# Kernel optimization log

Hardware: AMD Instinct MI355X
Metric: run time of the kernel (lower is better)

Reference implementation:

```python
import jax, jax.numpy as jnp
import numpy as np


def _iterative_pinv(mat, n_iter=6):
    # mat: [b, h, m, m]
    m = mat.shape[-1]
    I = jnp.eye(m, dtype=mat.dtype)
    # global (over all batch/heads) scaling, matching torch.max over full tensor
    init_coef = jnp.max(jnp.sum(jnp.abs(mat), axis=-2)) * jnp.max(jnp.sum(jnp.abs(mat), axis=-1))
    out = jnp.swapaxes(mat, -2, -1) / init_coef
    for _ in range(n_iter):
        mo = jnp.matmul(mat, out)          # [b,h,m,m]
        term1 = 7.0 * I - mo
        term2 = 15.0 * I - jnp.matmul(mo, term1)
        term3 = 13.0 * I - jnp.matmul(mo, term2)
        out = 0.25 * jnp.matmul(out, term3)
    return out


def _landmarks(x, m):
    # x: [b, h, s, d] -> segment means [b, h, m, d]
    b, h, s, d = x.shape
    l = s // m
    return x.reshape(b, h, m, l, d).mean(axis=-2)


def setup_inputs() -> dict:
    key = jax.random.key(0)
    kq, kk, kv = jax.random.split(key, 3)
    shape = (4, 12, 4096, 64)
    return {
        "query": jax.random.normal(kq, shape, dtype=jnp.float32),
        "key": jax.random.normal(kk, shape, dtype=jnp.float32),
        "value": jax.random.normal(kv, shape, dtype=jnp.float32),
        "num_landmarks": 64,
    }


def reference(query, key, value, num_landmarks):
    b, h, s, d = query.shape
    scale = 1.0 / jnp.sqrt(jnp.asarray(d, dtype=query.dtype))
    q_lm = _landmarks(query, num_landmarks)   # [b,h,m,d]
    k_lm = _landmarks(key, num_landmarks)     # [b,h,m,d]
    # F_tilde: [b,h,s,m]
    F_tilde = jax.nn.softmax(jnp.einsum('bhsd,bhmd->bhsm', query, k_lm) * scale, axis=-1)
    # A_tilde: pinv of [b,h,m,m]
    A_tilde = _iterative_pinv(
        jax.nn.softmax(jnp.einsum('bhnd,bhmd->bhnm', q_lm, k_lm) * scale, axis=-1))
    # B_tilde: [b,h,m,s]
    B_tilde = jax.nn.softmax(jnp.einsum('bhmd,bhsd->bhms', q_lm, key) * scale, axis=-1)
    # out = F_tilde @ (A_tilde @ (B_tilde @ value))  -> [b,h,s,d]
    bv = jnp.matmul(B_tilde, value)        # [b,h,m,d]
    abv = jnp.matmul(A_tilde, bv)          # [b,h,m,d]
    return jnp.matmul(F_tilde, abv)        # [b,h,s,d]
```

## Files before the change

### kernel.cpp

```cpp
#include <hip/hip_runtime.h>
#include <math.h>

#define BH 48
#define Ss 4096
#define Dd 64
#define Mm 64
#define NCH 16
#define SCALE 0.125f
#define PLN 4096

typedef unsigned int u32;
typedef unsigned short u16;
typedef __attribute__((ext_vector_type(8))) short short8;
typedef __attribute__((ext_vector_type(4))) float floatx4;

union FRAG { uint4 u; short8 s; };

#define MFMA(a,b,c) __builtin_amdgcn_mfma_f32_16x16x32_bf16(a,b,c,0,0,0)

__device__ __forceinline__ u32 pack2_hi(float a, float b) {
    return (__float_as_uint(a) >> 16) | (__float_as_uint(b) & 0xFFFF0000u);
}
__device__ __forceinline__ float trunc_bf(float a) {
    return __uint_as_float(__float_as_uint(a) & 0xFFFF0000u);
}
__device__ __forceinline__ void split1(float v, u16& h, u16& l) {
    u32 u = __float_as_uint(v);
    h = (u16)(u >> 16);
    float r = v - __uint_as_float(u & 0xFFFF0000u);
    l = (u16)(__float_as_uint(r) >> 16);
}
__device__ __forceinline__ void split8(const float* v, short8& h, short8& l) {
    FRAG H, L;
    float r[8];
#pragma unroll
    for (int i = 0; i < 8; i++) r[i] = v[i] - trunc_bf(v[i]);
    H.u.x = pack2_hi(v[0], v[1]); H.u.y = pack2_hi(v[2], v[3]);
    H.u.z = pack2_hi(v[4], v[5]); H.u.w = pack2_hi(v[6], v[7]);
    L.u.x = pack2_hi(r[0], r[1]); L.u.y = pack2_hi(r[2], r[3]);
    L.u.z = pack2_hi(r[4], r[5]); L.u.w = pack2_hi(r[6], r[7]);
    h = H.s; l = L.s;
}
__device__ __forceinline__ int swz(int row, int col) {
    return row * 64 + ((((col >> 3) ^ (row & 7)) << 3) | (col & 7));
}

__global__ __launch_bounds__(256) void k_landmarks(const float* __restrict__ Q,
                                                   const float* __restrict__ Kg,
                                                   float* __restrict__ qlm,
                                                   float* __restrict__ klm,
                                                   u16* __restrict__ qlmh, u16* __restrict__ qlml,
                                                   u16* __restrict__ klmh, u16* __restrict__ klml) {
    int g = blockIdx.x, bh = blockIdx.y;
    int t = threadIdx.x;
    int seg = t >> 4, d4 = t & 15;
    int m = g * 16 + seg;
    const float* src = blockIdx.z ? Kg : Q;
    float* dst = blockIdx.z ? klm : qlm;
    u16* dh = blockIdx.z ? klmh : qlmh;
    u16* dl = blockIdx.z ? klml : qlml;
    const float* base = src + ((size_t)bh * Ss + (size_t)m * 64) * Dd + d4 * 4;
    float4 acc = make_float4(0.f, 0.f, 0.f, 0.f);
#pragma unroll
    for (int l = 0; l < 64; l++) {
        float4 v = *(const float4*)(base + (size_t)l * Dd);
        acc.x += v.x; acc.y += v.y; acc.z += v.z; acc.w += v.w;
    }
    acc.x *= (1.f / 64.f); acc.y *= (1.f / 64.f);
    acc.z *= (1.f / 64.f); acc.w *= (1.f / 64.f);
    int idx = (bh * Mm + m) * Dd + d4 * 4;
    *(float4*)(dst + idx) = acc;
    float vv[4] = {acc.x, acc.y, acc.z, acc.w};
    u16 hh[4], ll[4];
#pragma unroll
    for (int i = 0; i < 4; i++) split1(vv[i], hh[i], ll[i]);
    *(uint2*)(dh + idx) = make_uint2((u32)hh[0] | ((u32)hh[1] << 16), (u32)hh[2] | ((u32)hh[3] << 16));
    *(uint2*)(dl + idx) = make_uint2((u32)ll[0] | ((u32)ll[1] << 16), (u32)ll[2] | ((u32)ll[3] << 16));
}

__global__ __launch_bounds__(256) void k_lmsm(const float* __restrict__ qlm,
                                              const float* __restrict__ klm,
                                              float* __restrict__ smat,
                                              unsigned int* __restrict__ coef) {
    int bh = blockIdx.x, t = threadIdx.x;
    __shared__ float kl[Mm * Dd];
    __shared__ float ql[Mm * Dd];
    __shared__ float Lp[Mm][Mm + 1];
    const float4* kb = (const float4*)(klm + bh * Mm * Dd);
    const float4* qb = (const float4*)(qlm + bh * Mm * Dd);
    for (int i = t; i < Mm * Dd / 4; i += 256) {
        ((float4*)kl)[i] = kb[i];
        ((float4*)ql)[i] = qb[i];
    }
    __syncthreads();
    int n = t >> 2, c = t & 3;
    float p[16];
#pragma unroll
    for (int jj = 0; jj < 16; jj++) {
        int m = c * 16 + jj;
        float s = 0.f;
#pragma unroll
        for (int d4 = 0; d4 < 16; d4++) {
            int d = (((d4 + c * 4) & 15)) * 4;
            float4 kv = *(const float4*)(kl + m * Dd + d);
            float4 qv = *(const float4*)(ql + n * Dd + d);
            s += qv.x * kv.x + qv.y * kv.y + qv.z * kv.z + qv.w * kv.w;
        }
        p[jj] = s * SCALE;
    }
    float mx = -INFINITY;
#pragma unroll
    for (int jj = 0; jj < 16; jj++) mx = fmaxf(mx, p[jj]);
    mx = fmaxf(mx, __shfl_xor(mx, 1));
    mx = fmaxf(mx, __shfl_xor(mx, 2));
    float den = 0.f;
#pragma unroll
    for (int jj = 0; jj < 16; jj++) { p[jj] = __expf(p[jj] - mx); den += p[jj]; }
    den += __shfl_xor(den, 1);
    den += __shfl_xor(den, 2);
    float inv = 1.0f / den;
#pragma unroll
    for (int jj = 0; jj < 16; jj++) Lp[n][c * 16 + jj] = p[jj] * inv;
    __syncthreads();
    float* sg = smat + bh * Mm * Mm;
    for (int i = t; i < Mm * Mm; i += 256) sg[i] = Lp[i >> 6][i & 63];
    if (t < Mm) {
        float cs = 0.f;
#pragma unroll
        for (int nn = 0; nn < Mm; nn++) cs += Lp[nn][t];
#pragma unroll
        for (int off = 1; off < 64; off <<= 1) cs = fmaxf(cs, __shfl_xor(cs, off));
        if (t == 0) atomicMax(coef + 0, __float_as_uint(cs));
    } else if (t < 2 * Mm) {
        int nn = t - Mm; float rs = 0.f;
#pragma unroll
        for (int m = 0; m < Mm; m++) rs += Lp[nn][m];
#pragma unroll
        for (int off = 1; off < 64; off <<= 1) rs = fmaxf(rs, __shfl_xor(rs, off));
        if (t == Mm) atomicMax(coef + 1, __float_as_uint(rs));
    }
}

__device__ __forceinline__ void pinv_pass(const u16* __restrict__ Ah, const u16* __restrict__ Al,
                                          const u16* __restrict__ Bph, const u16* __restrict__ Bpl,
                                          u16* __restrict__ Oh, u16* __restrict__ Ol,
                                          int w, int c, int hi,
                                          float diag, float sgn, float scl) {
    short8 bfh[2], bfl[2];
#pragma unroll
    for (int ks = 0; ks < 2; ks++) {
        bfh[ks] = *(const short8*)&Bph[swz(w * 16 + c, ks * 32 + hi * 8)];
        bfl[ks] = *(const short8*)&Bpl[swz(w * 16 + c, ks * 32 + hi * 8)];
    }
    int j = w * 16 + c;
#pragma unroll
    for (int ta = 0; ta < 4; ta++) {
        floatx4 acc = (floatx4){0.f, 0.f, 0.f, 0.f};
#pragma unroll
        for (int ks = 0; ks < 2; ks++) {
            short8 afh = *(const short8*)&Ah[swz(ta * 16 + c, ks * 32 + hi * 8)];
            short8 afl = *(const short8*)&Al[swz(ta * 16 + c, ks * 32 + hi * 8)];
            acc = MFMA(afh, bfh[ks], acc);
            acc = MFMA(afl, bfh[ks], acc);
            acc = MFMA(afh, bfl[ks], acc);
        }
        u16 oh[4], ol[4];
#pragma unroll
        for (int r = 0; r < 4; r++) {
            int i = ta * 16 + hi * 4 + r;
            float v = scl * (((i == j) ? diag : 0.f) + sgn * acc[r]);
            split1(v, oh[r], ol[r]);
        }
        int o0 = swz(j, ta * 16 + hi * 4);
        *(u32*)&Oh[o0]     = (u32)oh[0] | ((u32)oh[1] << 16);
        *(u32*)&Oh[o0 + 2] = (u32)oh[2] | ((u32)oh[3] << 16);
        *(u32*)&Ol[o0]     = (u32)ol[0] | ((u32)ol[1] << 16);
        *(u32*)&Ol[o0 + 2] = (u32)ol[2] | ((u32)ol[3] << 16);
    }
}

__global__ __launch_bounds__(256) void k_pinv(const float* __restrict__ smat,
                                              const unsigned int* __restrict__ coef,
                                              float* __restrict__ atil) {
    extern __shared__ u16 P[];
    u16* FaH  = P;             u16* FaL  = P + PLN;
    u16* FxcH = P + 2 * PLN;   u16* FxcL = P + 3 * PLN;
    u16* X0H  = P + 4 * PLN;   u16* X0L  = P + 5 * PLN;
    u16* X1H  = P + 6 * PLN;   u16* X1L  = P + 7 * PLN;
    u16* T1H  = P + 8 * PLN;   u16* T1L  = P + 9 * PLN;
    u16* T2H  = P + 10 * PLN;  u16* T2L  = P + 11 * PLN;
    int bh = blockIdx.x, t = threadIdx.x;
    int w = t >> 6, l = t & 63, c = l & 15, hi = l >> 4;
    float inv = 1.0f / (__uint_as_float(coef[0]) * __uint_as_float(coef[1]));
    {
        int r = t >> 2, kq = (t & 3) * 16;
        const float* ar = smat + bh * 4096 + r * 64 + kq;
        float v[16];
#pragma unroll
        for (int q = 0; q < 4; q++) {
            float4 x = *(const float4*)(ar + q * 4);
            v[q * 4 + 0] = x.x; v[q * 4 + 1] = x.y; v[q * 4 + 2] = x.z; v[q * 4 + 3] = x.w;
        }
        short8 h0, l0, h1, l1;
        split8(v, h0, l0); split8(v + 8, h1, l1);
        *(short8*)&FaH[swz(r, kq)] = h0;     *(short8*)&FaH[swz(r, kq + 8)] = h1;
        *(short8*)&FaL[swz(r, kq)] = l0;     *(short8*)&FaL[swz(r, kq + 8)] = l1;
        float vs[16];
#pragma unroll
        for (int q = 0; q < 16; q++) vs[q] = v[q] * inv;
        split8(vs, h0, l0); split8(vs + 8, h1, l1);
        *(short8*)&FxcH[swz(r, kq)] = h0;    *(short8*)&FxcH[swz(r, kq + 8)] = h1;
        *(short8*)&FxcL[swz(r, kq)] = l0;    *(short8*)&FxcL[swz(r, kq + 8)] = l1;
#pragma unroll
        for (int q = 0; q < 16; q++) {
            u16 h, lo; split1(vs[q], h, lo);
            X0H[swz(kq + q, r)] = h;
            X0L[swz(kq + q, r)] = lo;
        }
    }
    __syncthreads();
    u16 *xrH = X0H, *xrL = X0L, *moH = X1H, *moL = X1L;
    for (int it = 0; it < 6; it++) {
        pinv_pass(FxcH, FxcL, FaH, FaL, moH, moL, w, c, hi, 0.f, 1.f, 1.f);
        pinv_pass(FaH, FaL, FxcH, FxcL, T1H, T1L, w, c, hi, 7.f, -1.f, 1.f);
        __syncthreads();
        pinv_pass(moH, moL, T1H, T1L, T2H, T2L, w, c, hi, 15.f, -1.f, 1.f);
        __syncthreads();
        pinv_pass(moH, moL, T2H, T2L, T1H, T1L, w, c, hi, 13.f, -1.f, 1.f);
        __syncthreads();
        pinv_pass(T1H, T1L, xrH, xrL, moH, moL, w, c, hi, 0.f, 1.f, 0.25f);
        pinv_pass(xrH, xrL, T1H, T1L, FxcH, FxcL, w, c, hi, 0.f, 1.f, 0.25f);
        __syncthreads();
        u16* th = xrH; xrH = moH; moH = th;
        u16* tl = xrL; xrL = moL; moL = tl;
    }
    {
        int i = t >> 2, j0 = (t & 3) * 16;
        FRAG h0, l0, h1, l1;
        h0.s = *(const short8*)&xrH[swz(i, j0)];
        l0.s = *(const short8*)&xrL[swz(i, j0)];
        h1.s = *(const short8*)&xrH[swz(i, j0 + 8)];
        l1.s = *(const short8*)&xrL[swz(i, j0 + 8)];
        float* ob = atil + bh * 4096 + i * 64 + j0;
#pragma unroll
        for (int q = 0; q < 8; q++) {
            ob[q]     = __uint_as_float(((u32)(u16)h0.s[q]) << 16) + __uint_as_float(((u32)(u16)l0.s[q]) << 16);
            ob[q + 8] = __uint_as_float(((u32)(u16)h1.s[q]) << 16) + __uint_as_float(((u32)(u16)l1.s[q]) << 16);
        }
    }
}

__global__ __launch_bounds__(256) void k_bvp(const float* __restrict__ Kg,
                                             const float* __restrict__ Vg,
                                             const u16* __restrict__ qlmh,
                                             const u16* __restrict__ qlml,
                                             float* __restrict__ pnum,
                                             float* __restrict__ pden) {
    __shared__ __align__(16) u16 Pb[2][4096];
    __shared__ __align__(16) u16 vt[2][4096];
    __shared__ __align__(16) float tmp[64 * 68];
    int ch = blockIdx.x, bh = blockIdx.y;
    int t = threadIdx.x, w = t >> 6, l = t & 63, c = l & 15, hi = l >> 4;
    const float* Kbh = Kg + (size_t)bh * Ss * Dd;
    const float* Vbh = Vg + (size_t)bh * Ss * Dd;
    const u16* qh = qlmh + bh * Mm * Dd;
    const u16* ql = qlml + bh * Mm * Dd;
    floatx4 pvC[4];
    float denacc[16];
#pragma unroll
    for (int i = 0; i < 4; i++) pvC[i] = (floatx4){0.f, 0.f, 0.f, 0.f};
#pragma unroll
    for (int i = 0; i < 16; i++) denacc[i] = 0.f;

    for (int tile = 0; tile < 4; ++tile) {
        int s0 = ch * 256 + tile * 64;
        __syncthreads();
        {
            int sl = t >> 2, q = (t & 3) * 16;
            const float4* vp = (const float4*)(Vbh + (size_t)(s0 + sl) * Dd + q);
            float4* dp = (float4*)(tmp + sl * 68 + q);
#pragma unroll
            for (int qq = 0; qq < 4; qq++) dp[qq] = vp[qq];
        }
        {
            int srow = s0 + w * 16 + c;
            const float* kp = Kbh + (size_t)srow * Dd + hi * 8;
            short8 kbh[2], kbl[2];
#pragma unroll
            for (int ks = 0; ks < 2; ks++) {
                float kv[8];
                float4 a = *(const float4*)(kp + ks * 32);
                float4 b = *(const float4*)(kp + ks * 32 + 4);
                kv[0] = a.x; kv[1] = a.y; kv[2] = a.z; kv[3] = a.w;
                kv[4] = b.x; kv[5] = b.y; kv[6] = b.z; kv[7] = b.w;
                split8(kv, kbh[ks], kbl[ks]);
            }
            floatx4 qkC[4];
#pragma unroll
            for (int i = 0; i < 4; i++) qkC[i] = (floatx4){0.f, 0.f, 0.f, 0.f};
#pragma unroll
            for (int mt = 0; mt < 4; mt++) {
#pragma unroll
                for (int ks = 0; ks < 2; ks++) {
                    short8 aH = *(const short8*)&qh[(mt * 16 + c) * 64 + ks * 32 + hi * 8];
                    short8 aL = *(const short8*)&ql[(mt * 16 + c) * 64 + ks * 32 + hi * 8];
                    qkC[mt] = MFMA(aH, kbh[ks], qkC[mt]);
                    qkC[mt] = MFMA(aL, kbh[ks], qkC[mt]);
                    qkC[mt] = MFMA(aH, kbl[ks], qkC[mt]);
                }
            }
#pragma unroll
            for (int mt = 0; mt < 4; mt++) {
#pragma unroll
                for (int r = 0; r < 4; r++) {
                    float pv = __expf(qkC[mt][r] * SCALE);
                    denacc[mt * 4 + r] += pv;
                    int m = mt * 16 + hi * 4 + r;
                    u16 h, lo; split1(pv, h, lo);
                    Pb[0][swz(m, w * 16 + c)] = h;
                    Pb[1][swz(m, w * 16 + c)] = lo;
                }
            }
        }
        __syncthreads();
        {
            int d = t >> 2, sg = t & 3;
            float v[16];
#pragma unroll
            for (int j = 0; j < 16; j++) v[j] = tmp[(sg * 16 + j) * 68 + d];
            short8 h0, l0, h1, l1;
            split8(v, h0, l0); split8(v + 8, h1, l1);
            *(short8*)&vt[0][swz(d, sg * 16)] = h0;
            *(short8*)&vt[0][swz(d, sg * 16 + 8)] = h1;
            *(short8*)&vt[1][swz(d, sg * 16)] = l0;
            *(short8*)&vt[1][swz(d, sg * 16 + 8)] = l1;
        }
        __syncthreads();
#pragma unroll
        for (int ks = 0; ks < 2; ks++) {
            short8 pah = *(const short8*)&Pb[0][swz(w * 16 + c, ks * 32 + hi * 8)];
            short8 pal = *(const short8*)&Pb[1][swz(w * 16 + c, ks * 32 + hi * 8)];
#pragma unroll
            for (int dt = 0; dt < 4; dt++) {
                short8 vh = *(const short8*)&vt[0][swz(dt * 16 + c, ks * 32 + hi * 8)];
                short8 vl = *(const short8*)&vt[1][swz(dt * 16 + c, ks * 32 + hi * 8)];
                pvC[dt] = MFMA(pah, vh, pvC[dt]);
                pvC[dt] = MFMA(pal, vh, pvC[dt]);
                pvC[dt] = MFMA(pah, vl, pvC[dt]);
            }
        }
    }
    float* nb = pnum + (size_t)(bh * NCH + ch) * 4096;
#pragma unroll
    for (int dt = 0; dt < 4; dt++)
#pragma unroll
        for (int r = 0; r < 4; r++)
            nb[(w * 16 + hi * 4 + r) * 64 + dt * 16 + c] = pvC[dt][r];
#pragma unroll
    for (int i = 0; i < 16; i++) {
        float v = denacc[i];
        v += __shfl_xor(v, 1); v += __shfl_xor(v, 2);
        v += __shfl_xor(v, 4); v += __shfl_xor(v, 8);
        denacc[i] = v;
    }
    if (c == 0) {
        float* db = pden + (size_t)((bh * NCH + ch) * 4 + w) * 64;
#pragma unroll
        for (int mt = 0; mt < 4; mt++)
#pragma unroll
            for (int r = 0; r < 4; r++)
                db[mt * 16 + hi * 4 + r] = denacc[mt * 4 + r];
    }
}

__global__ __launch_bounds__(256) void k_bvc(const float* __restrict__ pnum,
                                             const float* __restrict__ pden,
                                             const float* __restrict__ atil,
                                             u16* __restrict__ abvh,
                                             u16* __restrict__ abvl) {
    int bh = blockIdx.x, t = threadIdx.x;
    __shared__ float bvs[Mm][Dd + 1];
    __shared__ float Ams[Mm * (Mm + 1)];
    const float* ab = atil + bh * Mm * Mm;
    for (int i = t; i < Mm * Mm; i += 256) Ams[(i >> 6) * 65 + (i & 63)] = ab[i];
    int m = t >> 2, c = t & 3, d0 = c * 16;
    float den = 0.f;
    const float* db = pden + (size_t)bh * NCH * 4 * 64;
#pragma unroll
    for (int i = 0; i < NCH * 4; i++) den += db[i * 64 + m];
    float acc[16];
#pragma unroll
    for (int i = 0; i < 16; i++) acc[i] = 0.f;
    const float* nb = pnum + (size_t)bh * NCH * 4096;
    for (int ch = 0; ch < NCH; ch++) {
        const float4* pa = (const float4*)(nb + ch * 4096 + m * 64 + d0);
#pragma unroll
        for (int q = 0; q < 4; q++) {
            float4 v = pa[q];
            acc[q * 4 + 0] += v.x; acc[q * 4 + 1] += v.y;
            acc[q * 4 + 2] += v.z; acc[q * 4 + 3] += v.w;
        }
    }
    float inv = 1.0f / den;
#pragma unroll
    for (int ii = 0; ii < 16; ii++) bvs[m][d0 + ii] = acc[ii] * inv;
    __syncthreads();
    int j = t & 63, i0 = (t >> 6) << 4;
    float outv[16];
#pragma unroll
    for (int ii = 0; ii < 16; ii++) outv[ii] = 0.f;
#pragma unroll
    for (int k = 0; k < Mm; k++) {
        float bk = bvs[k][j];
#pragma unroll
        for (int ii = 0; ii < 16; ii++) outv[ii] += Ams[(i0 + ii) * 65 + k] * bk;
    }
    u16* oh = abvh + bh * 4096;
    u16* ol = abvl + bh * 4096;
#pragma unroll
    for (int ii = 0; ii < 16; ii++) {
        u16 h, lo; split1(outv[ii], h, lo);
        oh[j * 64 + i0 + ii] = h;
        ol[j * 64 + i0 + ii] = lo;
    }
}

__global__ __launch_bounds__(256) void k_fout(const float* __restrict__ Qg,
                                              const u16* __restrict__ klmh,
                                              const u16* __restrict__ klml,
                                              const u16* __restrict__ abvh,
                                              const u16* __restrict__ abvl,
                                              float* __restrict__ Og) {
    __shared__ __align__(16) u16 Pw[4][2][1024];
    int st = blockIdx.x, bh = blockIdx.y;
    int t = threadIdx.x, w = t >> 6, l = t & 63, c = l & 15, hi = l >> 4;
    int srow = st * 64 + w * 16 + c;
    short8 qah[2], qal[2];
    {
        const float* qp = Qg + ((size_t)bh * Ss + srow) * Dd + hi * 8;
#pragma unroll
        for (int ks = 0; ks < 2; ks++) {
            float qv[8];
            float4 a = *(const float4*)(qp + ks * 32);
            float4 b = *(const float4*)(qp + ks * 32 + 4);
            qv[0] = a.x; qv[1] = a.y; qv[2] = a.z; qv[3] = a.w;
            qv[4] = b.x; qv[5] = b.y; qv[6] = b.z; qv[7] = b.w;
            split8(qv, qah[ks], qal[ks]);
        }
    }
    const u16* kh = klmh + bh * 4096;
    const u16* kl_ = klml + bh * 4096;
    floatx4 qkC[4];
#pragma unroll
    for (int i = 0; i < 4; i++) qkC[i] = (floatx4){0.f, 0.f, 0.f, 0.f};
#pragma unroll
    for (int mt = 0; mt < 4; mt++) {
#pragma unroll
        for (int ks = 0; ks < 2; ks++) {
            short8 bH = *(const short8*)&kh[(mt * 16 + c) * 64 + ks * 32 + hi * 8];
            short8 bL = *(const short8*)&kl_[(mt * 16 + c) * 64 + ks * 32 + hi * 8];
            qkC[mt] = MFMA(qah[ks], bH, qkC[mt]);
            qkC[mt] = MFMA(qal[ks], bH, qkC[mt]);
            qkC[mt] = MFMA(qah[ks], bL, qkC[mt]);
        }
    }
    float p[16], dsum[4];
#pragma unroll
    for (int r = 0; r < 4; r++) dsum[r] = 0.f;
#pragma unroll
    for (int mt = 0; mt < 4; mt++)
#pragma unroll
        for (int r = 0; r < 4; r++) {
            float pv = __expf(qkC[mt][r] * SCALE);
            p[mt * 4 + r] = pv;
            dsum[r] += pv;
        }
#pragma unroll
    for (int r = 0; r < 4; r++) {
        float v = dsum[r];
        v += __shfl_xor(v, 1); v += __shfl_xor(v, 2);
        v += __shfl_xor(v, 4); v += __shfl_xor(v, 8);
        dsum[r] = 1.0f / v;
    }
#pragma unroll
    for (int mt = 0; mt < 4; mt++)
#pragma unroll
        for (int r = 0; r < 4; r++) {
            float pv = p[mt * 4 + r] * dsum[r];
            u16 h, lo; split1(pv, h, lo);
            Pw[w][0][swz(hi * 4 + r, mt * 16 + c)] = h;
            Pw[w][1][swz(hi * 4 + r, mt * 16 + c)] = lo;
        }
    __syncthreads();
    short8 pah[2], pal[2];
#pragma unroll
    for (int ks = 0; ks < 2; ks++) {
        pah[ks] = *(const short8*)&Pw[w][0][swz(c, ks * 32 + hi * 8)];
        pal[ks] = *(const short8*)&Pw[w][1][swz(c, ks * 32 + hi * 8)];
    }
    const u16* ah = abvh + bh * 4096;
    const u16* al = abvl + bh * 4096;
    floatx4 oC[4];
#pragma unroll
    for (int i = 0; i < 4; i++) oC[i] = (floatx4){0.f, 0.f, 0.f, 0.f};
#pragma unroll
    for (int dt = 0; dt < 4; dt++) {
#pragma unroll
        for (int ks = 0; ks < 2; ks++) {
            short8 bH = *(const short8*)&ah[(dt * 16 + c) * 64 + ks * 32 + hi * 8];
            short8 bL = *(const short8*)&al[(dt * 16 + c) * 64 + ks * 32 + hi * 8];
            oC[dt] = MFMA(pah[ks], bH, oC[dt]);
            oC[dt] = MFMA(pal[ks], bH, oC[dt]);
            oC[dt] = MFMA(pah[ks], bL, oC[dt]);
        }
    }
    float* ob = Og + ((size_t)bh * Ss + st * 64 + w * 16) * Dd;
#pragma unroll
    for (int dt = 0; dt < 4; dt++)
#pragma unroll
        for (int r = 0; r < 4; r++)
            ob[(hi * 4 + r) * 64 + dt * 16 + c] = oC[dt][r];
}

extern "C" void kernel_launch(void* const* d_in, const int* in_sizes, int n_in,
                              void* d_out, int out_size, void* d_ws, size_t ws_size,
                              hipStream_t stream) {
    const float* Q = (const float*)d_in[0];
    const float* K = (const float*)d_in[1];
    const float* V = (const float*)d_in[2];
    float* out = (float*)d_out;
    float* ws = (float*)d_ws;
    unsigned int* coef = (unsigned int*)d_ws;
    float* qlm  = ws + 16;
    float* klm  = qlm  + BH * Mm * Dd;
    float* smat = klm  + BH * Mm * Dd;
    float* atil = smat + BH * Mm * Mm;
    float* pnum = atil + BH * Mm * Mm;
    float* pden = pnum + (size_t)BH * NCH * Mm * Dd;
    u16* ub   = (u16*)(pden + (size_t)BH * NCH * 4 * 64);
    u16* qlmh = ub;
    u16* qlml = qlmh + BH * Mm * Dd;
    u16* klmh = qlml + BH * Mm * Dd;
    u16* klml = klmh + BH * Mm * Dd;
    u16* abvh = klml + BH * Mm * Dd;
    u16* abvl = abvh + BH * Mm * Dd;

    hipMemsetAsync(d_ws, 0, 64, stream);

    k_landmarks<<<dim3(4, BH, 2), dim3(256), 0, stream>>>(Q, K, qlm, klm, qlmh, qlml, klmh, klml);
    k_lmsm<<<dim3(BH), dim3(256), 0, stream>>>(qlm, klm, smat, coef);
    k_pinv<<<dim3(BH), dim3(256), 12 * PLN * 2, stream>>>(smat, coef, atil);
    k_bvp<<<dim3(NCH, BH), dim3(256), 0, stream>>>(K, V, qlmh, qlml, pnum, pden);
    k_bvc<<<dim3(BH), dim3(256), 0, stream>>>(pnum, pden, atil, abvh, abvl);
    k_fout<<<dim3(Ss / 64, BH), dim3(256), 0, stream>>>(Q, klmh, klml, abvh, abvl, out);
}
```

Measured before the change: 175.4 us.

## Process two row tiles per k_fout block with prefetched Q and LDS barrier removal

k_fout now handles 128 sequence rows per block in two 64-row iterations. It prefetches the next tile's Q while the current tile computes. The block-wide __syncthreads is replaced with a per-wave lgkmcnt wait, which is valid because each wave only reads its own LDS slice. MFMA sections are wrapped in s_setprio. This halves the grid size, trading some parallelism for fewer block launches and overlapped Q loads.

```diff
diff --git a/kernel.cpp b/kernel.cpp
--- a/kernel.cpp
+++ b/kernel.cpp
@@ -432,94 +432,113 @@
                                               const u16* __restrict__ abvl,
                                               float* __restrict__ Og) {
     __shared__ __align__(16) u16 Pw[4][2][1024];
-    int st = blockIdx.x, bh = blockIdx.y;
+    int sb = blockIdx.x, bh = blockIdx.y;
     int t = threadIdx.x, w = t >> 6, l = t & 63, c = l & 15, hi = l >> 4;
-    int srow = st * 64 + w * 16 + c;
-    short8 qah[2], qal[2];
-    {
-        const float* qp = Qg + ((size_t)bh * Ss + srow) * Dd + hi * 8;
-#pragma unroll
-        for (int ks = 0; ks < 2; ks++) {
-            float qv[8];
-            float4 a = *(const float4*)(qp + ks * 32);
-            float4 b = *(const float4*)(qp + ks * 32 + 4);
-            qv[0] = a.x; qv[1] = a.y; qv[2] = a.z; qv[3] = a.w;
-            qv[4] = b.x; qv[5] = b.y; qv[6] = b.z; qv[7] = b.w;
-            split8(qv, qah[ks], qal[ks]);
-        }
-    }
     const u16* kh = klmh + bh * 4096;
     const u16* kl_ = klml + bh * 4096;
-    floatx4 qkC[4];
-#pragma unroll
-    for (int i = 0; i < 4; i++) qkC[i] = (floatx4){0.f, 0.f, 0.f, 0.f};
-#pragma unroll
-    for (int mt = 0; mt < 4; mt++) {
-#pragma unroll
-        for (int ks = 0; ks < 2; ks++) {
-            short8 bH = *(const short8*)&kh[(mt * 16 + c) * 64 + ks * 32 + hi * 8];
-            short8 bL = *(const short8*)&kl_[(mt * 16 + c) * 64 + ks * 32 + hi * 8];
-            qkC[mt] = MFMA(qah[ks], bH, qkC[mt]);
-            qkC[mt] = MFMA(qal[ks], bH, qkC[mt]);
-            qkC[mt] = MFMA(qah[ks], bL, qkC[mt]);
-        }
-    }
-    float p[16], dsum[4];
-#pragma unroll
-    for (int r = 0; r < 4; r++) dsum[r] = 0.f;
-#pragma unroll
-    for (int mt = 0; mt < 4; mt++)
-#pragma unroll
-        for (int r = 0; r < 4; r++) {
-            float pv = __expf(qkC[mt][r] * SCALE);
-            p[mt * 4 + r] = pv;
-            dsum[r] += pv;
-        }
-#pragma unroll
-    for (int r = 0; r < 4; r++) {
-        float v = dsum[r];
-        v += __shfl_xor(v, 1); v += __shfl_xor(v, 2);
-        v += __shfl_xor(v, 4); v += __shfl_xor(v, 8);
-        dsum[r] = 1.0f / v;
-    }
-#pragma unroll
-    for (int mt = 0; mt < 4; mt++)
-#pragma unroll
-        for (int r = 0; r < 4; r++) {
-            float pv = p[mt * 4 + r] * dsum[r];
-            u16 h, lo; split1(pv, h, lo);
-            Pw[w][0][swz(hi * 4 + r, mt * 16 + c)] = h;
-            Pw[w][1][swz(hi * 4 + r, mt * 16 + c)] = lo;
-        }
-    __syncthreads();
-    short8 pah[2], pal[2];
-#pragma unroll
-    for (int ks = 0; ks < 2; ks++) {
-        pah[ks] = *(const short8*)&Pw[w][0][swz(c, ks * 32 + hi * 8)];
-        pal[ks] = *(const short8*)&Pw[w][1][swz(c, ks * 32 + hi * 8)];
-    }
     const u16* ah = abvh + bh * 4096;
     const u16* al = abvl + bh * 4096;
-    floatx4 oC[4];
-#pragma unroll
-    for (int i = 0; i < 4; i++) oC[i] = (floatx4){0.f, 0.f, 0.f, 0.f};
-#pragma unroll
-    for (int dt = 0; dt < 4; dt++) {
+    const float* qbase = Qg + ((size_t)bh * Ss + (size_t)sb * 128 + w * 16 + c) * Dd + hi * 8;
+    float4 qv0[4];
+    qv0[0] = *(const float4*)(qbase + 0);
+    qv0[1] = *(const float4*)(qbase + 4);
+    qv0[2] = *(const float4*)(qbase + 32);
+    qv0[3] = *(const float4*)(qbase + 36);
+#pragma unroll
+    for (int ti = 0; ti < 2; ti++) {
+        float4 qn[4];
+        if (ti == 0) {
+            const float* q2 = qbase + 64 * Dd;
+            qn[0] = *(const float4*)(q2 + 0);
+            qn[1] = *(const float4*)(q2 + 4);
+            qn[2] = *(const float4*)(q2 + 32);
+            qn[3] = *(const float4*)(q2 + 36);
+        }
+        short8 qah[2], qal[2];
+        {
+            float qq[8];
+            qq[0] = qv0[0].x; qq[1] = qv0[0].y; qq[2] = qv0[0].z; qq[3] = qv0[0].w;
+            qq[4] = qv0[1].x; qq[5] = qv0[1].y; qq[6] = qv0[1].z; qq[7] = qv0[1].w;
+            split8(qq, qah[0], qal[0]);
+            qq[0] = qv0[2].x; qq[1] = qv0[2].y; qq[2] = qv0[2].z; qq[3] = qv0[2].w;
+            qq[4] = qv0[3].x; qq[5] = qv0[3].y; qq[6] = qv0[3].z; qq[7] = qv0[3].w;
+            split8(qq, qah[1], qal[1]);
+        }
+        floatx4 qkC[4];
+#pragma unroll
+        for (int i = 0; i < 4; i++) qkC[i] = (floatx4){0.f, 0.f, 0.f, 0.f};
+        __builtin_amdgcn_s_setprio(1);
+#pragma unroll
+        for (int mt = 0; mt < 4; mt++) {
+#pragma unroll
+            for (int ks = 0; ks < 2; ks++) {
+                short8 bH = *(const short8*)&kh[(mt * 16 + c) * 64 + ks * 32 + hi * 8];
+                short8 bL = *(const short8*)&kl_[(mt * 16 + c) * 64 + ks * 32 + hi * 8];
+                qkC[mt] = MFMA(qah[ks], bH, qkC[mt]);
+                qkC[mt] = MFMA(qal[ks], bH, qkC[mt]);
+                qkC[mt] = MFMA(qah[ks], bL, qkC[mt]);
+            }
+        }
+        __builtin_amdgcn_s_setprio(0);
+        float p[16], dsum[4];
+#pragma unroll
+        for (int r = 0; r < 4; r++) dsum[r] = 0.f;
+#pragma unroll
+        for (int mt = 0; mt < 4; mt++)
+#pragma unroll
+            for (int r = 0; r < 4; r++) {
+                float pv = __expf(qkC[mt][r] * SCALE);
+                p[mt * 4 + r] = pv;
+                dsum[r] += pv;
+            }
+#pragma unroll
+        for (int r = 0; r < 4; r++) {
+            float v = dsum[r];
+            v += __shfl_xor(v, 1); v += __shfl_xor(v, 2);
+            v += __shfl_xor(v, 4); v += __shfl_xor(v, 8);
+            dsum[r] = 1.0f / v;
+        }
+#pragma unroll
+        for (int mt = 0; mt < 4; mt++)
+#pragma unroll
+            for (int r = 0; r < 4; r++) {
+                float pv = p[mt * 4 + r] * dsum[r];
+                u16 h, lo; split1(pv, h, lo);
+                Pw[w][0][swz(hi * 4 + r, mt * 16 + c)] = h;
+                Pw[w][1][swz(hi * 4 + r, mt * 16 + c)] = lo;
+            }
+        asm volatile("s_waitcnt lgkmcnt(0)" ::: "memory");
+        __builtin_amdgcn_sched_barrier(0);
+        short8 pah[2], pal[2];
 #pragma unroll
         for (int ks = 0; ks < 2; ks++) {
-            short8 bH = *(const short8*)&ah[(dt * 16 + c) * 64 + ks * 32 + hi * 8];
-            short8 bL = *(const short8*)&al[(dt * 16 + c) * 64 + ks * 32 + hi * 8];
-            oC[dt] = MFMA(pah[ks], bH, oC[dt]);
-            oC[dt] = MFMA(pal[ks], bH, oC[dt]);
-            oC[dt] = MFMA(pah[ks], bL, oC[dt]);
-        }
-    }
-    float* ob = Og + ((size_t)bh * Ss + st * 64 + w * 16) * Dd;
-#pragma unroll
-    for (int dt = 0; dt < 4; dt++)
-#pragma unroll
-        for (int r = 0; r < 4; r++)
-            ob[(hi * 4 + r) * 64 + dt * 16 + c] = oC[dt][r];
+            pah[ks] = *(const short8*)&Pw[w][0][swz(c, ks * 32 + hi * 8)];
+            pal[ks] = *(const short8*)&Pw[w][1][swz(c, ks * 32 + hi * 8)];
+        }
+        floatx4 oC[4];
+#pragma unroll
+        for (int i = 0; i < 4; i++) oC[i] = (floatx4){0.f, 0.f, 0.f, 0.f};
+        __builtin_amdgcn_s_setprio(1);
+#pragma unroll
+        for (int dt = 0; dt < 4; dt++) {
+#pragma unroll
+            for (int ks = 0; ks < 2; ks++) {
+                short8 bH = *(const short8*)&ah[(dt * 16 + c) * 64 + ks * 32 + hi * 8];
+                short8 bL = *(const short8*)&al[(dt * 16 + c) * 64 + ks * 32 + hi * 8];
+                oC[dt] = MFMA(pah[ks], bH, oC[dt]);
+                oC[dt] = MFMA(pal[ks], bH, oC[dt]);
+                oC[dt] = MFMA(pah[ks], bL, oC[dt]);
+            }
+        }
+        __builtin_amdgcn_s_setprio(0);
+        float* ob = Og + ((size_t)bh * Ss + (size_t)sb * 128 + ti * 64 + w * 16) * Dd;
+#pragma unroll
+        for (int dt = 0; dt < 4; dt++)
+#pragma unroll
+            for (int r = 0; r < 4; r++)
+                ob[(hi * 4 + r) * 64 + dt * 16 + c] = oC[dt][r];
+        qv0[0] = qn[0]; qv0[1] = qn[1]; qv0[2] = qn[2]; qv0[3] = qn[3];
+    }
 }
 
 extern "C" void kernel_launch(void* const* d_in, const int* in_sizes, int n_in,
@@ -552,5 +571,5 @@
     k_pinv<<<dim3(BH), dim3(256), 12 * PLN * 2, stream>>>(smat, coef, atil);
     k_bvp<<<dim3(NCH, BH), dim3(256), 0, stream>>>(K, V, qlmh, qlml, pnum, pden);
     k_bvc<<<dim3(BH), dim3(256), 0, stream>>>(pnum, pden, atil, abvh, abvl);
-    k_fout<<<dim3(Ss / 64, BH), dim3(256), 0, stream>>>(Q, klmh, klml, abvh, abvl, out);
-}
+    k_fout<<<dim3(Ss / 128, BH), dim3(256), 0, stream>>>(Q, klmh, klml, abvh, abvl, out);
+}
```

Result: slower. 179.1 us (+2.1%).
